# Kernel tuning notes

Hardware: AMD Instinct MI355X
Metric: run time of the kernel (lower is better)

Reference implementation:

```python
import jax, jax.numpy as jnp
import numpy as np

B, T, C, U = 256, 512, 256, 64  # batch, time, classes (incl. blank), label length
BLANK = C - 1                   # keras ctc_batch_cost: blank is last class
S = 2 * U + 1                   # extended label length (blanks interleaved)
NEG = -1e30                     # safe log-zero for fp32
EPS = 1e-7                      # keras.backend.epsilon()


def setup_inputs() -> dict:
    key = jax.random.key(0)
    k1, k2 = jax.random.split(key)
    # y_pred are softmax probabilities over time, as fed to ctc_batch_cost
    y_pred = jax.nn.softmax(jax.random.normal(k1, (B, T, C), dtype=jnp.float32), axis=-1)
    # labels exclude the blank index (values in [0, C-2]); all U positions valid
    y_true = jax.random.randint(k2, (B, U), 0, C - 1, dtype=jnp.int32)
    return {"y_true": y_true, "y_pred": y_pred}


def _ctc_loss(y_pred, y_true):
    # keras ctc_batch_cost computes loss on log(y_pred + eps)
    log_probs = jnp.log(y_pred + EPS)                      # [B, T, C]
    # extended label sequence: blank, l1, blank, l2, ..., blank
    ext = jnp.full((B, S), BLANK, dtype=y_true.dtype).at[:, 1::2].set(y_true)
    # gather per-state emission log-probs: lp_ext[b,t,s] = log_probs[b,t,ext[b,s]]
    lp_ext = jnp.take_along_axis(log_probs, ext[:, None, :].astype(jnp.int32), axis=2)  # [B,T,S]
    # skip transition (s-2 -> s) allowed iff ext[s] != blank and ext[s] != ext[s-2]
    ext_m2 = jnp.pad(ext[:, :-2], ((0, 0), (2, 0)), constant_values=-1)
    skip_ok = (ext != BLANK) & (ext != ext_m2)             # [B, S]

    # alpha_0: can start in state 0 (blank) or state 1 (first label)
    alpha0 = (jnp.full((B, S), NEG, dtype=jnp.float32)
              .at[:, 0].set(lp_ext[:, 0, 0])
              .at[:, 1].set(lp_ext[:, 0, 1]))

    def step(alpha, lp_t):
        a1 = jnp.pad(alpha[:, :-1], ((0, 0), (1, 0)), constant_values=NEG)
        a2 = jnp.pad(alpha[:, :-2], ((0, 0), (2, 0)), constant_values=NEG)
        a2 = jnp.where(skip_ok, a2, NEG)
        alpha = jnp.logaddexp(jnp.logaddexp(alpha, a1), a2) + lp_t
        return alpha, None

    lp_time_major = jnp.swapaxes(lp_ext, 0, 1)             # [T, B, S]
    alpha, _ = jax.lax.scan(step, alpha0, lp_time_major[1:])
    # terminate in last blank or last label
    loss = -jnp.logaddexp(alpha[:, -1], alpha[:, -2])      # [B]
    return loss[:, None]                                   # [B, 1] like ctc_batch_cost


def reference(y_true, y_pred):
    return _ctc_loss(y_pred, y_true)
```

## Files before the change

### kernel.cpp

```cpp
#include <hip/hip_runtime.h>


constexpr int B = 256, T = 512, C = 256, U = 64;
constexpr int CH = 16;
#define EPSF 1e-7f

typedef float f4 __attribute__((ext_vector_type(4)));

#define LDSA(p) ((unsigned)(size_t)(__attribute__((address_space(3))) void*)(p))

__device__ __forceinline__ float dpp_wave_shr1(float x) {
    return __int_as_float(__builtin_amdgcn_update_dpp(
        0, __float_as_int(x), 0x138, 0xf, 0xf, true));
}

#define DPPMAX(ctrl)                                                      \
    {                                                                     \
        float x_ = __int_as_float(__builtin_amdgcn_update_dpp(            \
            0, __float_as_int(m_), (ctrl), 0xf, 0xf, true));              \
        m_ = fmaxf(m_, x_);                                               \
    }

#define RESCALE()                                                         \
    {                                                                     \
        float m_ = fmaxf(fmaxf(a_even, a_odd), a_top);                    \
        DPPMAX(0x111) DPPMAX(0x112) DPPMAX(0x114) DPPMAX(0x118)           \
        DPPMAX(0x142) DPPMAX(0x143)                                       \
        const float mx_ = __int_as_float(                                 \
            __builtin_amdgcn_readlane(__float_as_int(m_), 63));           \
        int e_ = (__float_as_int(mx_) >> 23) & 0xff;                      \
        int k_ = 187 - e_;                                                \
        k_ = k_ > 127 ? 127 : k_;                                         \
        const float s_ = __int_as_float((k_ + 127) << 23);                \
        a_even *= s_; a_odd *= s_; a_top *= s_;                           \
        esum += k_;                                                       \
    }

#define GLD(dst, p)                                                        \
    asm volatile("global_load_dwordx4 %0, %1, off" : "=&v"(dst) : "v"(p));

#define ISSUE(cc, ST)                                                      \
    {                                                                      \
        const int c_ = (cc);                                               \
        _Pragma("unroll")                                                  \
        for (int j = 0; j < 4; ++j) {                                      \
            int t = 1 + c_ * CH + rbase + j;                               \
            t = t < T ? t : T - 1;                                         \
            const float* g_ = rowp + t * C + (lane << 2);                  \
            GLD(ST[j], g_)                                                 \
        }                                                                  \
    }

#define WRITE4(ST, WB)                                                     \
    asm volatile("ds_write_b128 %0, %1" :: "v"(WB), "v"(ST[0]));           \
    asm volatile("ds_write_b128 %0, %1 offset:1024" :: "v"(WB), "v"(ST[1]));\
    asm volatile("ds_write_b128 %0, %1 offset:2048" :: "v"(WB), "v"(ST[2]));\
    asm volatile("ds_write_b128 %0, %1 offset:3072" :: "v"(WB), "v"(ST[3]));

#define VMC(N)                                                             \
    asm volatile("s_waitcnt vmcnt(" #N ")" ::: "memory");                  \
    __builtin_amdgcn_sched_barrier(0);

#define DSR(dst, addr, OS)                                                 \
    asm volatile("ds_read_b32 %0, %1 offset:" OS                           \
                 : "=v"(dst) : "v"(addr));

#define GATHER(LA, BA)                                                     \
    {                                                                      \
        DSR(lab[0],  LA, "0")     DSR(lab[1],  LA, "1024")                 \
        DSR(lab[2],  LA, "2048")  DSR(lab[3],  LA, "3072")                 \
        DSR(lab[4],  LA, "4096")  DSR(lab[5],  LA, "5120")                 \
        DSR(lab[6],  LA, "6144")  DSR(lab[7],  LA, "7168")                 \
        DSR(lab[8],  LA, "8192")  DSR(lab[9],  LA, "9216")                 \
        DSR(lab[10], LA, "10240") DSR(lab[11], LA, "11264")                \
        DSR(lab[12], LA, "12288") DSR(lab[13], LA, "13312")                \
        DSR(lab[14], LA, "14336") DSR(lab[15], LA, "15360")                \
        DSR(blk[0],  BA, "0")     DSR(blk[1],  BA, "1024")                 \
        DSR(blk[2],  BA, "2048")  DSR(blk[3],  BA, "3072")                 \
        DSR(blk[4],  BA, "4096")  DSR(blk[5],  BA, "5120")                 \
        DSR(blk[6],  BA, "6144")  DSR(blk[7],  BA, "7168")                 \
        DSR(blk[8],  BA, "8192")  DSR(blk[9],  BA, "9216")                 \
        DSR(blk[10], BA, "10240") DSR(blk[11], BA, "11264")                \
        DSR(blk[12], BA, "12288") DSR(blk[13], BA, "13312")                \
        DSR(blk[14], BA, "14336") DSR(blk[15], BA, "15360")                \
    }

#define FENCE_BAR()                                                        \
    asm volatile("s_waitcnt lgkmcnt(0)" ::: "memory");                     \
    __builtin_amdgcn_sched_barrier(0);                                     \
    __builtin_amdgcn_s_barrier();

#define COMP_CHUNK(NSTEPS)                                                 \
    {                                                                      \
        _Pragma("unroll")                                                  \
        for (int i = 0; i < (NSTEPS); ++i) {                               \
            const float pb = blk[i] + EPSF;                                \
            const float pl = lab[i] + EPSF;                                \
            const float po = dpp_wave_shr1(a_odd);                         \
            const float skp = skip_ok ? po : 0.f;                          \
            const float ne = (a_even + po) * pb;                           \
            const float no = (a_odd + a_even + skp) * pl;                  \
            const float nt = (a_top + a_odd) * pb;                         \
            a_even = ne; a_odd = no; a_top = nt;                           \
            if (((1 + i) & 7) == 0) RESCALE();                             \
        }                                                                  \
    }

#define ITER(cc, STI, STW, WB, LA, BA)                                     \
    {                                                                      \
        if (wid == 0) { GATHER(LA, BA) }                                   \
        __builtin_amdgcn_sched_barrier(0);                                 \
        ISSUE((cc) + 4, STI)                                               \
        VMC(12)                                                            \
        WRITE4(STW, WB)                                                    \
        FENCE_BAR()                                                        \
        if (wid == 0) { COMP_CHUNK(CH) }                                   \
    }

#define ITER_T(cc, NN, STW, WB, LA, BA)                                    \
    {                                                                      \
        if (wid == 0) { GATHER(LA, BA) }                                   \
        __builtin_amdgcn_sched_barrier(0);                                 \
        VMC(NN)                                                            \
        WRITE4(STW, WB)                                                    \
        FENCE_BAR()                                                        \
        if (wid == 0) { COMP_CHUNK(CH) }                                   \
    }

__global__ __launch_bounds__(256) void ctc_kernel(const int* __restrict__ y_true,
                                                  const float* __restrict__ y_pred,
                                                  float* __restrict__ out) {
    __shared__ float rows[2][CH][C];
    const int b = blockIdx.x;
    const int tid = threadIdx.x;
    const int lane = tid & 63;
    const int wid = tid >> 6;
    const int rbase = wid << 2;
    const float* __restrict__ rowp = y_pred + (size_t)b * (T * C);

    const int label = y_true[b * U + lane];
    const int label_prev = __shfl_up(label, 1);
    const bool skip_ok = (lane > 0) && (label != label_prev);

    float a_even = 0.f, a_odd = 0.f, a_top = 0.f;
    int esum = 0;
    float lab[CH], blk[CH];

    if (wid == 0) {
        const float pb = rowp[C - 1] + EPSF;
        const float pl = rowp[label] + EPSF;
        a_even = (lane == 0) ? pb : 0.f;
        a_odd  = (lane == 0) ? pl : 0.f;
    }

    const unsigned wb0 = LDSA(&rows[0][rbase][0]) + (lane << 4);
    const unsigned wb1 = LDSA(&rows[1][rbase][0]) + (lane << 4);
    const unsigned labA0 = LDSA(&rows[0][0][label]);
    const unsigned labA1 = LDSA(&rows[1][0][label]);
    const unsigned blkA0 = LDSA(&rows[0][0][C - 1]);
    const unsigned blkA1 = LDSA(&rows[1][0][C - 1]);

    f4 s0[4], s1[4], s2[4], s3[4];

    asm volatile("s_waitcnt vmcnt(0)" ::: "memory");
    __builtin_amdgcn_sched_barrier(0);

    ISSUE(0, s0) ISSUE(1, s1) ISSUE(2, s2) ISSUE(3, s3)
    VMC(12)
    WRITE4(s0, wb0)
    FENCE_BAR()

    for (int q = 0; q < 7; ++q) {
        const int c = q << 2;
        ITER(c + 0, s0, s1, wb1, labA0, blkA0)
        ITER(c + 1, s1, s2, wb0, labA1, blkA1)
        ITER(c + 2, s2, s3, wb1, labA0, blkA0)
        ITER(c + 3, s3, s0, wb0, labA1, blkA1)
    }
    ITER_T(28, 8, s1, wb1, labA0, blkA0)
    ITER_T(29, 4, s2, wb0, labA1, blkA1)
    ITER_T(30, 0, s3, wb1, labA0, blkA0)

    if (wid == 0) {
        GATHER(labA1, blkA1)
        asm volatile("s_waitcnt lgkmcnt(0)" ::: "memory");
        __builtin_amdgcn_sched_barrier(0);
        COMP_CHUNK(CH - 1)
        if (lane == 63)
            out[b] = -logf(a_top + a_odd) + (float)esum * 0.69314718055994531f;
    }
}

extern "C" void kernel_launch(void* const* d_in, const int* in_sizes, int n_in,
                              void* d_out, int out_size, void* d_ws, size_t ws_size,
                              hipStream_t stream) {
    const int* y_true   = (const int*)d_in[0];
    const float* y_pred = (const float*)d_in[1];
    float* out = (float*)d_out;
    hipLaunchKernelGGL(ctc_kernel, dim3(B), dim3(256), 0, stream,
                       y_true, y_pred, out);
}
```

Measured before the change: 195.5 us.

## Split CTC recursion into forward and backward halves with combine kernel

Each batch row is now handled by two blocks: one runs the alpha (forward) recursion over the first half of time, the other runs the beta (backward) recursion over the second half. Their state vectors are written to workspace and a small second kernel combines them with a dot product. This halves the serial dependency chain and doubles the block count. It also replaces register-staged loads plus LDS writes with direct global-to-LDS loads in a 4-deep ring buffer. The costs are a second kernel launch, a workspace round trip, and extra DPP shifts in the backward step.

```diff
diff --git a/kernel.cpp b/kernel.cpp
--- a/kernel.cpp
+++ b/kernel.cpp
@@ -3,15 +3,20 @@
 
 constexpr int B = 256, T = 512, C = 256, U = 64;
 constexpr int CH = 16;
+constexpr int NCH = 16;
+constexpr int WSH = 130;
+constexpr int WSB = 260;
 #define EPSF 1e-7f
-
-typedef float f4 __attribute__((ext_vector_type(4)));
 
 #define LDSA(p) ((unsigned)(size_t)(__attribute__((address_space(3))) void*)(p))
 
 __device__ __forceinline__ float dpp_wave_shr1(float x) {
     return __int_as_float(__builtin_amdgcn_update_dpp(
         0, __float_as_int(x), 0x138, 0xf, 0xf, true));
+}
+__device__ __forceinline__ float dpp_wave_shl1(float x) {
+    return __int_as_float(__builtin_amdgcn_update_dpp(
+        0, __float_as_int(x), 0x130, 0xf, 0xf, true));
 }
 
 #define DPPMAX(ctrl)                                                      \
@@ -36,30 +41,20 @@
         esum += k_;                                                       \
     }
 
-#define GLD(dst, p)                                                        \
-    asm volatile("global_load_dwordx4 %0, %1, off" : "=&v"(dst) : "v"(p));
-
-#define ISSUE(cc, ST)                                                      \
-    {                                                                      \
-        const int c_ = (cc);                                               \
+#define STAGE_W(cc, RT)                                                    \
+    {                                                                      \
+        float* lbase_ = &rows[(cc) & 3][0][0];                             \
         _Pragma("unroll")                                                  \
         for (int j = 0; j < 4; ++j) {                                      \
-            int t = 1 + c_ * CH + rbase + j;                               \
-            t = t < T ? t : T - 1;                                         \
-            const float* g_ = rowp + t * C + (lane << 2);                  \
-            GLD(ST[j], g_)                                                 \
+            const int i_ = rbase + j;                                      \
+            const int t_ = (RT) + i_;                                      \
+            const float* g_ = rowp + t_ * C + (lane << 2);                 \
+            __builtin_amdgcn_global_load_lds(                              \
+                (const __attribute__((address_space(1))) void*)g_,         \
+                (__attribute__((address_space(3))) void*)(lbase_ + i_ * C),\
+                16, 0, 0);                                                 \
         }                                                                  \
     }
-
-#define WRITE4(ST, WB)                                                     \
-    asm volatile("ds_write_b128 %0, %1" :: "v"(WB), "v"(ST[0]));           \
-    asm volatile("ds_write_b128 %0, %1 offset:1024" :: "v"(WB), "v"(ST[1]));\
-    asm volatile("ds_write_b128 %0, %1 offset:2048" :: "v"(WB), "v"(ST[2]));\
-    asm volatile("ds_write_b128 %0, %1 offset:3072" :: "v"(WB), "v"(ST[3]));
-
-#define VMC(N)                                                             \
-    asm volatile("s_waitcnt vmcnt(" #N ")" ::: "memory");                  \
-    __builtin_amdgcn_sched_barrier(0);
 
 #define DSR(dst, addr, OS)                                                 \
     asm volatile("ds_read_b32 %0, %1 offset:" OS                           \
@@ -85,15 +80,18 @@
         DSR(blk[14], BA, "14336") DSR(blk[15], BA, "15360")                \
     }
 
-#define FENCE_BAR()                                                        \
+#define LGKM_FENCE()                                                       \
     asm volatile("s_waitcnt lgkmcnt(0)" ::: "memory");                     \
-    __builtin_amdgcn_sched_barrier(0);                                     \
-    __builtin_amdgcn_s_barrier();
-
-#define COMP_CHUNK(NSTEPS)                                                 \
-    {                                                                      \
-        _Pragma("unroll")                                                  \
-        for (int i = 0; i < (NSTEPS); ++i) {                               \
+    __builtin_amdgcn_sched_barrier(0);
+
+#define VMC(N)                                                             \
+    asm volatile("s_waitcnt vmcnt(" #N ")" ::: "memory");                  \
+    __builtin_amdgcn_sched_barrier(0);
+
+#define COMP_FWD()                                                         \
+    {                                                                      \
+        _Pragma("unroll")                                                  \
+        for (int i = 0; i < CH; ++i) {                                     \
             const float pb = blk[i] + EPSF;                                \
             const float pl = lab[i] + EPSF;                                \
             const float po = dpp_wave_shr1(a_odd);                         \
@@ -106,88 +104,145 @@
         }                                                                  \
     }
 
-#define ITER(cc, STI, STW, WB, LA, BA)                                     \
-    {                                                                      \
-        if (wid == 0) { GATHER(LA, BA) }                                   \
-        __builtin_amdgcn_sched_barrier(0);                                 \
-        ISSUE((cc) + 4, STI)                                               \
-        VMC(12)                                                            \
-        WRITE4(STW, WB)                                                    \
-        FENCE_BAR()                                                        \
-        if (wid == 0) { COMP_CHUNK(CH) }                                   \
-    }
-
-#define ITER_T(cc, NN, STW, WB, LA, BA)                                    \
-    {                                                                      \
-        if (wid == 0) { GATHER(LA, BA) }                                   \
-        __builtin_amdgcn_sched_barrier(0);                                 \
-        VMC(NN)                                                            \
-        WRITE4(STW, WB)                                                    \
-        FENCE_BAR()                                                        \
-        if (wid == 0) { COMP_CHUNK(CH) }                                   \
-    }
-
-__global__ __launch_bounds__(256) void ctc_kernel(const int* __restrict__ y_true,
-                                                  const float* __restrict__ y_pred,
-                                                  float* __restrict__ out) {
-    __shared__ float rows[2][CH][C];
-    const int b = blockIdx.x;
-    const int tid = threadIdx.x;
-    const int lane = tid & 63;
-    const int wid = tid >> 6;
+#define BSTEP(i, DO_R)                                                     \
+    {                                                                      \
+        const float pb = blk[i] + EPSF;                                    \
+        const float pl = lab[i] + EPSF;                                    \
+        const float se = dpp_wave_shl1(a_even);                            \
+        const float so = dpp_wave_shl1(a_odd);                             \
+        const float fu = (lane == 63) ? a_top : se;                        \
+        const float ne = (a_even + a_odd) * pb;                            \
+        const float no = (a_odd + fu + (sk_next ? so : 0.f)) * pl;         \
+        const float nt = a_top * pb;                                       \
+        a_even = ne; a_odd = no; a_top = nt;                               \
+        if (DO_R) RESCALE();                                               \
+    }
+
+#define COMP_BWD_FIRST()                                                   \
+    {                                                                      \
+        a_odd  = (lane == 63) ? lab[15] + EPSF : 0.f;                      \
+        a_top  = blk[15] + EPSF;                                           \
+        a_even = 0.f;                                                      \
+        _Pragma("unroll")                                                  \
+        for (int i = 14; i >= 0; --i) BSTEP(i, (i == 8) || (i == 0))       \
+    }
+#define COMP_BWD_MID()                                                     \
+    {                                                                      \
+        _Pragma("unroll")                                                  \
+        for (int i = 15; i >= 0; --i) BSTEP(i, (i == 8) || (i == 0))       \
+    }
+#define COMP_BWD_LAST()                                                    \
+    {                                                                      \
+        _Pragma("unroll")                                                  \
+        for (int i = 15; i >= 1; --i) BSTEP(i, (i == 8))                   \
+        const float se = dpp_wave_shl1(a_even);                            \
+        const float so = dpp_wave_shl1(a_odd);                             \
+        const float fu = (lane == 63) ? a_top : se;                        \
+        const float ye = a_even + a_odd;                                   \
+        const float yo = a_odd + fu + (sk_next ? so : 0.f);                \
+        a_even = ye; a_odd = yo;                                           \
+    }
+
+#define DO_COMP(cc)                                                        \
+    if (half) {                                                            \
+        if ((cc) == 0) { COMP_BWD_FIRST() } else { COMP_BWD_MID() }        \
+    } else { COMP_FWD() }
+
+__global__ __launch_bounds__(256) void ctc_half(const int* __restrict__ y_true,
+                                                const float* __restrict__ y_pred,
+                                                float* __restrict__ ws) {
+    __shared__ float rows[4][CH][C];
+    const int bid = blockIdx.x;
+    const int b = bid >> 1, half = bid & 1;
+    const int tid = threadIdx.x, lane = tid & 63, wid = tid >> 6;
     const int rbase = wid << 2;
     const float* __restrict__ rowp = y_pred + (size_t)b * (T * C);
 
     const int label = y_true[b * U + lane];
     const int label_prev = __shfl_up(label, 1);
+    const int label_next = __shfl_down(label, 1);
     const bool skip_ok = (lane > 0) && (label != label_prev);
+    const bool sk_next = (lane < 63) && (label_next != label);
 
     float a_even = 0.f, a_odd = 0.f, a_top = 0.f;
     int esum = 0;
     float lab[CH], blk[CH];
 
-    if (wid == 0) {
+    if (half == 0 && wid == 0) {
         const float pb = rowp[C - 1] + EPSF;
         const float pl = rowp[label] + EPSF;
         a_even = (lane == 0) ? pb : 0.f;
         a_odd  = (lane == 0) ? pl : 0.f;
     }
 
-    const unsigned wb0 = LDSA(&rows[0][rbase][0]) + (lane << 4);
-    const unsigned wb1 = LDSA(&rows[1][rbase][0]) + (lane << 4);
-    const unsigned labA0 = LDSA(&rows[0][0][label]);
-    const unsigned labA1 = LDSA(&rows[1][0][label]);
-    const unsigned blkA0 = LDSA(&rows[0][0][C - 1]);
-    const unsigned blkA1 = LDSA(&rows[1][0][C - 1]);
-
-    f4 s0[4], s1[4], s2[4], s3[4];
+    const unsigned labB = LDSA(&rows[0][0][label]);
+    const unsigned blkB = LDSA(&rows[0][0][C - 1]);
+    const int rt0 = half ? 496 : 1;
+    const int rts = half ? -16 : 16;
 
     asm volatile("s_waitcnt vmcnt(0)" ::: "memory");
     __builtin_amdgcn_sched_barrier(0);
 
-    ISSUE(0, s0) ISSUE(1, s1) ISSUE(2, s2) ISSUE(3, s3)
-    VMC(12)
-    WRITE4(s0, wb0)
-    FENCE_BAR()
-
-    for (int q = 0; q < 7; ++q) {
-        const int c = q << 2;
-        ITER(c + 0, s0, s1, wb1, labA0, blkA0)
-        ITER(c + 1, s1, s2, wb0, labA1, blkA1)
-        ITER(c + 2, s2, s3, wb1, labA0, blkA0)
-        ITER(c + 3, s3, s0, wb0, labA1, blkA1)
-    }
-    ITER_T(28, 8, s1, wb1, labA0, blkA0)
-    ITER_T(29, 4, s2, wb0, labA1, blkA1)
-    ITER_T(30, 0, s3, wb1, labA0, blkA0)
-
+    STAGE_W(0, rt0)
+    STAGE_W(1, rt0 + rts)
+    STAGE_W(2, rt0 + 2 * rts)
+    VMC(8)
+    __builtin_amdgcn_s_barrier();
+
+    for (int c = 0; c < 13; ++c) {
+        const unsigned off = (unsigned)(c & 3) << 14;
+        if (wid == 0) { GATHER(labB + off, blkB + off) }
+        __builtin_amdgcn_sched_barrier(0);
+        STAGE_W(c + 3, rt0 + (c + 3) * rts)
+        if (wid == 0) {
+            LGKM_FENCE();
+            DO_COMP(c)
+        }
+        VMC(8)
+        __builtin_amdgcn_s_barrier();
+    }
     if (wid == 0) {
-        GATHER(labA1, blkA1)
-        asm volatile("s_waitcnt lgkmcnt(0)" ::: "memory");
-        __builtin_amdgcn_sched_barrier(0);
-        COMP_CHUNK(CH - 1)
-        if (lane == 63)
-            out[b] = -logf(a_top + a_odd) + (float)esum * 0.69314718055994531f;
+        GATHER(labB + (1u << 14), blkB + (1u << 14))
+        LGKM_FENCE();
+        DO_COMP(13)
+    }
+    VMC(4)
+    __builtin_amdgcn_s_barrier();
+    if (wid == 0) {
+        GATHER(labB + (2u << 14), blkB + (2u << 14))
+        LGKM_FENCE();
+        DO_COMP(14)
+    }
+    VMC(0)
+    __builtin_amdgcn_s_barrier();
+    if (wid == 0) {
+        GATHER(labB + (3u << 14), blkB + (3u << 14))
+        LGKM_FENCE();
+        if (half) { COMP_BWD_LAST() } else { COMP_FWD() }
+        float* wp = ws + b * WSB + half * WSH;
+        wp[lane] = a_even;
+        wp[64 + lane] = a_odd;
+        if (lane == 63) {
+            wp[128] = a_top;
+            wp[129] = (float)esum;
+        }
+    }
+}
+
+__global__ __launch_bounds__(64) void ctc_combine(const float* __restrict__ ws,
+                                                  float* __restrict__ out) {
+    const int b = blockIdx.x;
+    const int l = threadIdx.x;
+    const float* fp = ws + b * WSB;
+    const float* bp = fp + WSH;
+    double s = (double)fp[l] * (double)bp[l] +
+               (double)fp[64 + l] * (double)bp[64 + l];
+    if (l == 63) s += (double)fp[128] * (double)bp[128];
+    for (int off = 32; off; off >>= 1) s += __shfl_xor(s, off);
+    if (l == 0) {
+        const float ef = fp[129], eb = bp[129];
+        out[b] = (float)(-log(s) +
+                         (double)(ef + eb) * 0.6931471805599453);
     }
 }
 
@@ -197,6 +252,8 @@
     const int* y_true   = (const int*)d_in[0];
     const float* y_pred = (const float*)d_in[1];
     float* out = (float*)d_out;
-    hipLaunchKernelGGL(ctc_kernel, dim3(B), dim3(256), 0, stream,
-                       y_true, y_pred, out);
-}
+    float* ws  = (float*)d_ws;
+    hipLaunchKernelGGL(ctc_half, dim3(2 * B), dim3(256), 0, stream,
+                       y_true, y_pred, ws);
+    hipLaunchKernelGGL(ctc_combine, dim3(B), dim3(64), 0, stream, ws, out);
+}
```

New measurement: 195.6 us. No clear change (+0.0%).
